# Performance work log

Hardware: AMD Instinct MI355X
Metric: run time of the kernel (lower is better)

## Reference

```python
import jax, jax.numpy as jnp
import numpy as np

N_NODES = 50000
N_EDGES = 800000
N_OBS = 4
HID = 64
K_HOPS = 5


def setup_inputs() -> dict:
    key = jax.random.key(0)
    ks = jax.random.split(key, 8)
    nodes = jax.random.normal(ks[0], (N_NODES, N_OBS), dtype=jnp.float32)
    edge_src = jax.random.randint(ks[1], (N_EDGES,), 0, N_NODES, dtype=jnp.int32)
    edge_dst = jax.random.randint(ks[2], (N_EDGES,), 0, N_NODES, dtype=jnp.int32)
    edge_weight = jax.random.uniform(ks[3], (N_EDGES,), dtype=jnp.float32)
    # Linear weights stored as (in, out); y = x @ W + b
    W_lift = jax.random.normal(ks[4], (1, HID), dtype=jnp.float32) * 0.5
    b_lift = jax.random.normal(ks[5], (HID,), dtype=jnp.float32) * 0.1
    W_hop = jax.random.normal(ks[6], (HID, HID), dtype=jnp.float32) * (1.0 / np.sqrt(HID))
    b_hop = jax.random.normal(ks[7], (HID,), dtype=jnp.float32) * 0.1
    return {"nodes": nodes, "edge_src": edge_src, "edge_dst": edge_dst,
            "edge_weight": edge_weight, "W_lift": W_lift, "b_lift": b_lift,
            "W_hop": W_hop, "b_hop": b_hop}


def reference(nodes, edge_src, edge_dst, edge_weight, W_lift, b_lift, W_hop, b_hop):
    # lift: (N, O, 1) @ (1, H) + b -> (N, O, H)
    X = nodes[:, :, None] @ W_lift + b_lift

    def hop(X, _):
        # sparse adjacency matmul: agg[d] = sum_{e: dst=d} w_e * X[src_e]
        msgs = edge_weight[:, None, None] * X[edge_src]          # (E, O, H)
        agg = jax.ops.segment_sum(msgs, edge_dst, num_segments=N_NODES)
        # shared Linear (torch [Linear]*k aliases one module) + ReLU
        return jax.nn.relu(agg @ W_hop + b_hop), None

    X, _ = jax.lax.scan(hop, X, None, length=K_HOPS)
    return X  # (N_NODES, N_OBS, HID)
```

## Files before the change

### kernel.cpp

```cpp
#include <hip/hip_runtime.h>
#include <hip/hip_fp16.h>

#define N_NODES 50000
#define N_EDGES 800000
#define N_OBS   4
#define HID     64
#define K_HOPS  5
#define ROW     (N_OBS * HID)
#define NSCAN_BLKS ((N_NODES + 1023) / 1024)

typedef _Float16 f16x8 __attribute__((ext_vector_type(8)));
typedef _Float16 f16x4 __attribute__((ext_vector_type(4)));
typedef float    f32x4 __attribute__((ext_vector_type(4)));

__global__ void zero_kernel(int* __restrict__ p, int n) {
    int i = blockIdx.x * blockDim.x + threadIdx.x;
    if (i < n) p[i] = 0;
}

__global__ void hist_kernel(const int* __restrict__ dst, int* __restrict__ cnt,
                            int* __restrict__ erank) {
    int e = blockIdx.x * blockDim.x + threadIdx.x;
    if (e < N_EDGES) erank[e] = atomicAdd(&cnt[dst[e]], 1);
}

__global__ __launch_bounds__(1024) void scan1_kernel(const int* __restrict__ counts,
                                                     int* __restrict__ bsum) {
    __shared__ int wsum[16];
    const int t = threadIdx.x, lane = t & 63, wid = t >> 6;
    int i = blockIdx.x * 1024 + t;
    int x = (i < N_NODES) ? counts[i] : 0;
    #pragma unroll
    for (int off = 32; off > 0; off >>= 1) x += __shfl_xor(x, off);
    if (lane == 0) wsum[wid] = x;
    __syncthreads();
    if (t == 0) {
        int s = 0;
        #pragma unroll
        for (int j = 0; j < 16; ++j) s += wsum[j];
        bsum[blockIdx.x] = s;
    }
}

__global__ void scan2_kernel(int* __restrict__ bsum) {
    const int t = threadIdx.x;
    int v = (t < NSCAN_BLKS) ? bsum[t] : 0;
    int x = v;
    #pragma unroll
    for (int off = 1; off < 64; off <<= 1) {
        int y = __shfl_up(x, off);
        if (t >= off) x += y;
    }
    if (t < NSCAN_BLKS) bsum[t] = x - v;
}

__global__ __launch_bounds__(1024) void scan3_kernel(const int* __restrict__ counts,
                                                     const int* __restrict__ bsum,
                                                     int* __restrict__ offsets) {
    __shared__ int wsum[16];
    __shared__ int wpre[16];
    const int t = threadIdx.x, lane = t & 63, wid = t >> 6;
    int i = blockIdx.x * 1024 + t;
    int v = (i < N_NODES) ? counts[i] : 0;
    int x = v;
    #pragma unroll
    for (int off = 1; off < 64; off <<= 1) {
        int y = __shfl_up(x, off);
        if (lane >= off) x += y;
    }
    if (lane == 63) wsum[wid] = x;
    __syncthreads();
    if (t < 16) {
        int p = 0;
        for (int j = 0; j < t; ++j) p += wsum[j];
        wpre[t] = p;
    }
    __syncthreads();
    int base = bsum[blockIdx.x];
    int incl = base + x + wpre[wid];
    if (i < N_NODES) offsets[i + 1] = incl;
    if (i == 0) offsets[0] = 0;
}

__global__ void scatter_kernel(const int* __restrict__ src, const int* __restrict__ dst,
                               const float* __restrict__ w, const int* __restrict__ offsets,
                               const int* __restrict__ erank,
                               unsigned int* __restrict__ ecmp) {
    int e = blockIdx.x * blockDim.x + threadIdx.x;
    if (e < N_EDGES) {
        int d = dst[e];
        int p = offsets[d] + erank[e];
        __half hw = __float2half(w[e]);
        ecmp[p] = ((unsigned int)__half_as_ushort(hw) << 16) | (unsigned int)src[e];
    }
}

__global__ void packW_kernel(const float* __restrict__ W, _Float16* __restrict__ Bp) {
    int i = blockIdx.x * 256 + threadIdx.x;
    if (i >= 4096) return;
    int j  = i & 7;
    int l  = (i >> 3) & 63;
    int ks = (i >> 9) & 1;
    int w  = i >> 10;
    int k   = ks * 32 + ((j >> 2) * 16) + ((l >> 4) * 4) + (j & 3);
    int col = w * 16 + (l & 15);
    Bp[i] = (_Float16)W[k * 64 + col];
}

__global__ void wlw_kernel(const float* __restrict__ Wl, const float* __restrict__ bl,
                           const float* __restrict__ W, float* __restrict__ WlW,
                           float* __restrict__ blW) {
    int j = threadIdx.x;
    float a = 0.f, b = 0.f;
    #pragma unroll 8
    for (int h = 0; h < 64; ++h) {
        float wv = W[h * 64 + j];
        a += Wl[h] * wv;
        b += bl[h] * wv;
    }
    WlW[j] = a;
    blW[j] = b;
}

__global__ void hop1_gather_kernel(const int* __restrict__ offsets,
                                   const unsigned int* __restrict__ ecmp,
                                   const float* __restrict__ nodes,
                                   float4* __restrict__ T, float* __restrict__ U) {
    int n = blockIdx.x * blockDim.x + threadIdx.x;
    if (n >= N_NODES) return;
    int s = offsets[n], e = offsets[n + 1];
    float4 t = {0.f, 0.f, 0.f, 0.f};
    float u = 0.f;
    for (int i = s; i < e; ++i) {
        unsigned int p = ecmp[i];
        float w = __half2float(__ushort_as_half((unsigned short)(p >> 16)));
        int sn = (int)(p & 0xffffu);
        float4 nv = ((const float4*)nodes)[sn];
        t.x += w * nv.x; t.y += w * nv.y; t.z += w * nv.z; t.w += w * nv.w;
        u += w;
    }
    T[n] = t;
    U[n] = u;
}

__global__ void hop1_finish_kernel(const float4* __restrict__ T, const float* __restrict__ U,
                                   const float* __restrict__ WlW, const float* __restrict__ blW,
                                   const float* __restrict__ bias, __half* __restrict__ X) {
    int i = blockIdx.x * blockDim.x + threadIdx.x;
    const int total = N_NODES * ROW / 4;
    if (i >= total) return;
    int n   = i >> 6;
    int rem = i & 63;
    int o   = rem >> 4;
    int h4  = rem & 15;
    float t = ((const float*)&T[n])[o];
    float u = U[n];
    float4 wv = ((const float4*)WlW)[h4];
    float4 bv = ((const float4*)blW)[h4];
    float4 hv = ((const float4*)bias)[h4];
    f16x4 st;
    st[0] = (_Float16)fmaxf(t * wv.x + u * bv.x + hv.x, 0.f);
    st[1] = (_Float16)fmaxf(t * wv.y + u * bv.y + hv.y, 0.f);
    st[2] = (_Float16)fmaxf(t * wv.z + u * bv.z + hv.z, 0.f);
    st[3] = (_Float16)fmaxf(t * wv.w + u * bv.w + hv.w, 0.f);
    *(f16x4*)(X + (size_t)i * 4) = st;
}

template<int LAST>
__global__ __launch_bounds__(256) void hop_kernel(const int* __restrict__ offsets,
                                                  const unsigned int* __restrict__ ecmp,
                                                  const __half* __restrict__ Xin,
                                                  const _Float16* __restrict__ Bp,
                                                  const float* __restrict__ bias,
                                                  __half* __restrict__ Xout,
                                                  float* __restrict__ Fout) {
    __shared__ _Float16 As16[16][72];
    const int t = threadIdx.x;
    const int wid = t >> 6, lane = t & 63;
    const int half = lane >> 5;
    const int l32 = lane & 31;
    const int node = blockIdx.x * 4 + wid;
    const int s = offsets[node], e = offsets[node + 1];
    const _Float16* __restrict__ X16 = (const _Float16*)Xin;

    f16x8 acc0 = (f16x8)(_Float16)0.0f;
    f16x8 acc1 = (f16x8)(_Float16)0.0f;

    for (int base = s; base < e; base += 64) {
        int cnt = e - base;
        if (cnt > 64) cnt = 64;
        unsigned int pk = 0u;
        if (lane < cnt) pk = ecmp[base + lane];
        int pairs  = (cnt + 1) >> 1;
        int pairs8 = (pairs + 7) & ~7;
        for (int pb = 0; pb < pairs8; pb += 8) {
            f16x8 r[8];
            _Float16 wh[8];
            #pragma unroll
            for (int q = 0; q < 8; ++q) {
                int sl = 2 * (pb + q) + half;
                unsigned int p = (unsigned int)__shfl((int)pk, sl);
                unsigned short wu = (unsigned short)(p >> 16);
                wh[q] = __builtin_bit_cast(_Float16, wu);
                int idx = (int)(p & 0xffffu) * ROW;
                r[q] = *(const f16x8*)(X16 + idx + l32 * 8);
            }
            #pragma unroll
            for (int q = 0; q < 8; q += 2) {
                acc0 += r[q]     * wh[q];
                acc1 += r[q + 1] * wh[q + 1];
            }
        }
    }
    acc0 += acc1;

    int4 ai = *(int4*)&acc0;
    int4 bi;
    bi.x = __shfl_xor(ai.x, 32);
    bi.y = __shfl_xor(ai.y, 32);
    bi.z = __shfl_xor(ai.z, 32);
    bi.w = __shfl_xor(ai.w, 32);
    acc0 += *(f16x8*)&bi;

    if (half == 0) {
        int o = l32 >> 3, kb = (l32 & 7) * 8;
        *(f16x8*)&As16[wid * 4 + o][kb] = acc0;
    }
    __syncthreads();

    const int r15 = lane & 15;
    const int g   = lane >> 4;
    f16x8 a0, a1;
    ((f16x4*)&a0)[0] = *(const f16x4*)&As16[r15][ 0 + 4 * g];
    ((f16x4*)&a0)[1] = *(const f16x4*)&As16[r15][16 + 4 * g];
    ((f16x4*)&a1)[0] = *(const f16x4*)&As16[r15][32 + 4 * g];
    ((f16x4*)&a1)[1] = *(const f16x4*)&As16[r15][48 + 4 * g];
    f16x8 b0 = *(const f16x8*)(Bp + ((size_t)(wid * 2 + 0) * 64 + lane) * 8);
    f16x8 b1 = *(const f16x8*)(Bp + ((size_t)(wid * 2 + 1) * 64 + lane) * 8);
    f32x4 c = {0.f, 0.f, 0.f, 0.f};
    c = __builtin_amdgcn_mfma_f32_16x16x32_f16(a0, b0, c, 0, 0, 0);
    c = __builtin_amdgcn_mfma_f32_16x16x32_f16(a1, b1, c, 0, 0, 0);

    const float bv = bias[wid * 16 + r15];
    const size_t obase = (size_t)(blockIdx.x * 4 + g) * ROW + wid * 16 + r15;
    #pragma unroll
    for (int j = 0; j < 4; ++j) {
        float v = fmaxf(c[j] + bv, 0.f);
        if (LAST) Fout[obase + j * 64] = v;
        else      Xout[obase + j * 64] = __float2half(v);
    }
}

extern "C" void kernel_launch(void* const* d_in, const int* in_sizes, int n_in,
                              void* d_out, int out_size, void* d_ws, size_t ws_size,
                              hipStream_t stream) {
    const float* nodes   = (const float*)d_in[0];
    const int*   esrc    = (const int*)d_in[1];
    const int*   edst    = (const int*)d_in[2];
    const float* eweight = (const float*)d_in[3];
    const float* W_lift  = (const float*)d_in[4];
    const float* b_lift  = (const float*)d_in[5];
    const float* W_hop   = (const float*)d_in[6];
    const float* b_hop   = (const float*)d_in[7];

    char* ws = (char*)d_ws;
    __half*       X0   = (__half*)(ws);
    __half*       X1   = (__half*)(ws + 25600000);
    unsigned int* ECMP = (unsigned int*)(ws + 51200000);
    int*          OFF  = (int*)(ws + 54400000);
    int*          CNT  = (int*)(ws + 54600064);
    int*          BSUM = (int*)(ws + 54800064);
    _Float16*     BP   = (_Float16*)(ws + 54800320);
    float*        WLW  = (float*)(ws + 54808512);
    float*        BLW  = (float*)(ws + 54808768);
    int*          ERANK = (int*)(ws + 54809024);
    float4*       T    = (float4*)(ws + 54809024);
    float*        U    = (float*)(ws + 55609024);

    zero_kernel<<<(N_NODES + 255) / 256, 256, 0, stream>>>(CNT, N_NODES);
    hist_kernel<<<(N_EDGES + 255) / 256, 256, 0, stream>>>(edst, CNT, ERANK);
    scan1_kernel<<<NSCAN_BLKS, 1024, 0, stream>>>(CNT, BSUM);
    scan2_kernel<<<1, 64, 0, stream>>>(BSUM);
    scan3_kernel<<<NSCAN_BLKS, 1024, 0, stream>>>(CNT, BSUM, OFF);
    scatter_kernel<<<(N_EDGES + 255) / 256, 256, 0, stream>>>(esrc, edst, eweight, OFF, ERANK, ECMP);

    packW_kernel<<<16, 256, 0, stream>>>(W_hop, BP);
    wlw_kernel<<<1, 64, 0, stream>>>(W_lift, b_lift, W_hop, WLW, BLW);

    hop1_gather_kernel<<<(N_NODES + 255) / 256, 256, 0, stream>>>(OFF, ECMP, nodes, T, U);
    hop1_finish_kernel<<<(N_NODES * ROW / 4 + 255) / 256, 256, 0, stream>>>(T, U, WLW, BLW, b_hop, X0);

    const int hopGrid = N_NODES / 4;
    __half* Xi = X0;
    __half* Xo = X1;
    for (int hop = 1; hop < K_HOPS; ++hop) {
        if (hop == K_HOPS - 1) {
            hop_kernel<1><<<hopGrid, 256, 0, stream>>>(OFF, ECMP, Xi, BP, b_hop,
                                                       nullptr, (float*)d_out);
        } else {
            hop_kernel<0><<<hopGrid, 256, 0, stream>>>(OFF, ECMP, Xi, BP, b_hop,
                                                       Xo, nullptr);
        }
        __half* tmp = Xi; Xi = Xo; Xo = tmp;
    }
}
```

Before: 309.0 us.

## Split node features into per-observation planes and pin each plane to an XCD pair

```diff
diff --git a/kernel.cpp b/kernel.cpp
--- a/kernel.cpp
+++ b/kernel.cpp
@@ -145,7 +145,7 @@
 
 __global__ void hop1_finish_kernel(const float4* __restrict__ T, const float* __restrict__ U,
                                    const float* __restrict__ WlW, const float* __restrict__ blW,
-                                   const float* __restrict__ bias, __half* __restrict__ X) {
+                                   const float* __restrict__ bias, _Float16* __restrict__ X) {
     int i = blockIdx.x * blockDim.x + threadIdx.x;
     const int total = N_NODES * ROW / 4;
     if (i >= total) return;
@@ -163,91 +163,92 @@
     st[1] = (_Float16)fmaxf(t * wv.y + u * bv.y + hv.y, 0.f);
     st[2] = (_Float16)fmaxf(t * wv.z + u * bv.z + hv.z, 0.f);
     st[3] = (_Float16)fmaxf(t * wv.w + u * bv.w + hv.w, 0.f);
-    *(f16x4*)(X + (size_t)i * 4) = st;
+    *(f16x4*)(X + ((size_t)o * N_NODES + n) * 64 + h4 * 4) = st;
 }
 
 template<int LAST>
 __global__ __launch_bounds__(256) void hop_kernel(const int* __restrict__ offsets,
                                                   const unsigned int* __restrict__ ecmp,
-                                                  const __half* __restrict__ Xin,
+                                                  const _Float16* __restrict__ Xin,
                                                   const _Float16* __restrict__ Bp,
                                                   const float* __restrict__ bias,
-                                                  __half* __restrict__ Xout,
+                                                  _Float16* __restrict__ Xout,
                                                   float* __restrict__ Fout) {
-    __shared__ _Float16 As16[16][72];
+    __shared__ _Float16 As[32][72];
     const int t = threadIdx.x;
     const int wid = t >> 6, lane = t & 63;
-    const int half = lane >> 5;
-    const int l32 = lane & 31;
-    const int node = blockIdx.x * 4 + wid;
-    const int s = offsets[node], e = offsets[node + 1];
-    const _Float16* __restrict__ X16 = (const _Float16*)Xin;
+    const int b = blockIdx.x;
+    const int xcd = b & 7;
+    const int o = xcd >> 1;
+    const int g = ((b >> 3) << 1) | (xcd & 1);
+    const int n0 = g * 32;
+    if (n0 >= N_NODES) return;
+
+    const int g8  = lane >> 3;
+    const int sub = lane & 7;
+    const int local = wid * 8 + g8;
+    const int node = n0 + local;
+    const int nc = (node < N_NODES) ? node : N_NODES - 1;
+    int sN = offsets[nc];
+    int eN = offsets[nc + 1];
+    if (node >= N_NODES) eN = sN;
+
+    const _Float16* __restrict__ Xb = Xin + (size_t)o * (N_NODES * 64);
 
     f16x8 acc0 = (f16x8)(_Float16)0.0f;
     f16x8 acc1 = (f16x8)(_Float16)0.0f;
-
-    for (int base = s; base < e; base += 64) {
-        int cnt = e - base;
-        if (cnt > 64) cnt = 64;
-        unsigned int pk = 0u;
-        if (lane < cnt) pk = ecmp[base + lane];
-        int pairs  = (cnt + 1) >> 1;
-        int pairs8 = (pairs + 7) & ~7;
-        for (int pb = 0; pb < pairs8; pb += 8) {
-            f16x8 r[8];
-            _Float16 wh[8];
-            #pragma unroll
-            for (int q = 0; q < 8; ++q) {
-                int sl = 2 * (pb + q) + half;
-                unsigned int p = (unsigned int)__shfl((int)pk, sl);
-                unsigned short wu = (unsigned short)(p >> 16);
-                wh[q] = __builtin_bit_cast(_Float16, wu);
-                int idx = (int)(p & 0xffffu) * ROW;
-                r[q] = *(const f16x8*)(X16 + idx + l32 * 8);
-            }
-            #pragma unroll
-            for (int q = 0; q < 8; q += 2) {
-                acc0 += r[q]     * wh[q];
-                acc1 += r[q + 1] * wh[q + 1];
+    int i = sN;
+    for (; i + 2 <= eN; i += 2) {
+        unsigned int p0 = ecmp[i];
+        unsigned int p1 = ecmp[i + 1];
+        _Float16 w0 = __builtin_bit_cast(_Float16, (unsigned short)(p0 >> 16));
+        _Float16 w1 = __builtin_bit_cast(_Float16, (unsigned short)(p1 >> 16));
+        int s0 = (int)(p0 & 0xffffu) * 64;
+        int s1 = (int)(p1 & 0xffffu) * 64;
+        f16x8 r0 = *(const f16x8*)(Xb + s0 + sub * 8);
+        f16x8 r1 = *(const f16x8*)(Xb + s1 + sub * 8);
+        acc0 += r0 * w0;
+        acc1 += r1 * w1;
+    }
+    if (i < eN) {
+        unsigned int p0 = ecmp[i];
+        _Float16 w0 = __builtin_bit_cast(_Float16, (unsigned short)(p0 >> 16));
+        int s0 = (int)(p0 & 0xffffu) * 64;
+        f16x8 r0 = *(const f16x8*)(Xb + s0 + sub * 8);
+        acc0 += r0 * w0;
+    }
+    acc0 += acc1;
+    *(f16x8*)&As[local][sub * 8] = acc0;
+    __syncthreads();
+
+    const int r15 = lane & 15, gq = lane >> 4;
+    const int nt  = wid >> 1;
+    const int ct0 = (wid & 1) * 2;
+    const int arow = nt * 16 + r15;
+    f16x8 a0, a1;
+    ((f16x4*)&a0)[0] = *(const f16x4*)&As[arow][ 0 + 4 * gq];
+    ((f16x4*)&a0)[1] = *(const f16x4*)&As[arow][16 + 4 * gq];
+    ((f16x4*)&a1)[0] = *(const f16x4*)&As[arow][32 + 4 * gq];
+    ((f16x4*)&a1)[1] = *(const f16x4*)&As[arow][48 + 4 * gq];
+    #pragma unroll
+    for (int c = 0; c < 2; ++c) {
+        const int ct = ct0 + c;
+        f16x8 b0 = *(const f16x8*)(Bp + ((size_t)(ct * 2 + 0) * 64 + lane) * 8);
+        f16x8 b1 = *(const f16x8*)(Bp + ((size_t)(ct * 2 + 1) * 64 + lane) * 8);
+        f32x4 cc = {0.f, 0.f, 0.f, 0.f};
+        cc = __builtin_amdgcn_mfma_f32_16x16x32_f16(a0, b0, cc, 0, 0, 0);
+        cc = __builtin_amdgcn_mfma_f32_16x16x32_f16(a1, b1, cc, 0, 0, 0);
+        const int h = ct * 16 + r15;
+        const float bv = bias[h];
+        #pragma unroll
+        for (int j = 0; j < 4; ++j) {
+            int nj = n0 + nt * 16 + gq * 4 + j;
+            if (nj < N_NODES) {
+                float v = fmaxf(cc[j] + bv, 0.f);
+                if (LAST) Fout[(size_t)nj * ROW + o * 64 + h] = v;
+                else      Xout[((size_t)o * N_NODES + nj) * 64 + h] = (_Float16)v;
             }
         }
-    }
-    acc0 += acc1;
-
-    int4 ai = *(int4*)&acc0;
-    int4 bi;
-    bi.x = __shfl_xor(ai.x, 32);
-    bi.y = __shfl_xor(ai.y, 32);
-    bi.z = __shfl_xor(ai.z, 32);
-    bi.w = __shfl_xor(ai.w, 32);
-    acc0 += *(f16x8*)&bi;
-
-    if (half == 0) {
-        int o = l32 >> 3, kb = (l32 & 7) * 8;
-        *(f16x8*)&As16[wid * 4 + o][kb] = acc0;
-    }
-    __syncthreads();
-
-    const int r15 = lane & 15;
-    const int g   = lane >> 4;
-    f16x8 a0, a1;
-    ((f16x4*)&a0)[0] = *(const f16x4*)&As16[r15][ 0 + 4 * g];
-    ((f16x4*)&a0)[1] = *(const f16x4*)&As16[r15][16 + 4 * g];
-    ((f16x4*)&a1)[0] = *(const f16x4*)&As16[r15][32 + 4 * g];
-    ((f16x4*)&a1)[1] = *(const f16x4*)&As16[r15][48 + 4 * g];
-    f16x8 b0 = *(const f16x8*)(Bp + ((size_t)(wid * 2 + 0) * 64 + lane) * 8);
-    f16x8 b1 = *(const f16x8*)(Bp + ((size_t)(wid * 2 + 1) * 64 + lane) * 8);
-    f32x4 c = {0.f, 0.f, 0.f, 0.f};
-    c = __builtin_amdgcn_mfma_f32_16x16x32_f16(a0, b0, c, 0, 0, 0);
-    c = __builtin_amdgcn_mfma_f32_16x16x32_f16(a1, b1, c, 0, 0, 0);
-
-    const float bv = bias[wid * 16 + r15];
-    const size_t obase = (size_t)(blockIdx.x * 4 + g) * ROW + wid * 16 + r15;
-    #pragma unroll
-    for (int j = 0; j < 4; ++j) {
-        float v = fmaxf(c[j] + bv, 0.f);
-        if (LAST) Fout[obase + j * 64] = v;
-        else      Xout[obase + j * 64] = __float2half(v);
     }
 }
 
@@ -264,8 +265,8 @@
     const float* b_hop   = (const float*)d_in[7];
 
     char* ws = (char*)d_ws;
-    __half*       X0   = (__half*)(ws);
-    __half*       X1   = (__half*)(ws + 25600000);
+    _Float16*     X0   = (_Float16*)(ws);
+    _Float16*     X1   = (_Float16*)(ws + 25600000);
     unsigned int* ECMP = (unsigned int*)(ws + 51200000);
     int*          OFF  = (int*)(ws + 54400000);
     int*          CNT  = (int*)(ws + 54600064);
@@ -290,9 +291,9 @@
     hop1_gather_kernel<<<(N_NODES + 255) / 256, 256, 0, stream>>>(OFF, ECMP, nodes, T, U);
     hop1_finish_kernel<<<(N_NODES * ROW / 4 + 255) / 256, 256, 0, stream>>>(T, U, WLW, BLW, b_hop, X0);
 
-    const int hopGrid = N_NODES / 4;
-    __half* Xi = X0;
-    __half* Xo = X1;
+    const int hopGrid = 8 * 782;
+    _Float16* Xi = X0;
+    _Float16* Xo = X1;
     for (int hop = 1; hop < K_HOPS; ++hop) {
         if (hop == K_HOPS - 1) {
             hop_kernel<1><<<hopGrid, 256, 0, stream>>>(OFF, ECMP, Xi, BP, b_hop,
@@ -301,6 +302,6 @@
             hop_kernel<0><<<hopGrid, 256, 0, stream>>>(OFF, ECMP, Xi, BP, b_hop,
                                                        Xo, nullptr);
         }
-        __half* tmp = Xi; Xi = Xo; Xo = tmp;
-    }
-}
+        _Float16* tmp = Xi; Xi = Xo; Xo = tmp;
+    }
+}
```

New measurement: 313.0 us. About the same (+1.3%).
